# Kernel optimization log

Measured on AMD Instinct MI355X. Metric: run time of the kernel, lower is better.

Reference implementation:

```python
import jax, jax.numpy as jnp
import numpy as np

H, Mdim, C, P = 24, 48, 8, 8  # h = h_tilde, m = m_tilde, m_control, p


def setup_inputs() -> dict:
    key = jax.random.key(0)
    k = jax.random.split(key, 7)
    return {
        "y_rev": jax.random.normal(k[0], (2 * Mdim, P, 1), dtype=jnp.float32),  # y_rev[s] = y_nat_history[-(s+1)]
        "M_tilde": jax.random.normal(k[1], (H, Mdim, C, P), dtype=jnp.float32),
        "M": jax.random.normal(k[2], (H, Mdim, H, Mdim, C, P), dtype=jnp.float32),
        "sigma": jax.random.uniform(k[3], (H,), dtype=jnp.float32),      # positive Hankel eigenvalues
        "lambda_e": jax.random.uniform(k[4], (H,), dtype=jnp.float32),   # positive Hankel eigenvalues
        "phi": jax.random.normal(k[5], (Mdim, H), dtype=jnp.float32),
        "phi_tilde": jax.random.normal(k[6], (Mdim, H), dtype=jnp.float32),
    }


def reference(y_rev, M_tilde, M, sigma, lambda_e, phi, phi_tilde):
    m = phi.shape[0]
    lam4 = lambda_e ** 0.25  # [h]
    sig4 = sigma ** 0.25     # [h]
    y_m = y_rev[:m]          # [m, p, 1], y_m[j] = y_nat_history[-(j+1)]

    # term 0: M_tilde[0,0] @ y_t^nat
    u = M_tilde[0, 0] @ y_rev[0]  # [c, 1]

    # term 1: sum_ij lambda_i^{1/4} phi[j,i] (M_tilde[i,j] @ y_{t-j})
    c2 = lam4[:, None] * phi.T  # [h, m]
    u = u + jnp.einsum("ij,ijcp,jpq->cq", c2, M_tilde, y_m)

    # term 2: sum_lk sigma_l^{1/4} phi_tilde[k,l] (M[l,k,0,0] @ y_{t-k})
    c3 = sig4[:, None] * phi_tilde.T  # [h, m]
    u = u + jnp.einsum("lk,lkcp,kpq->cq", c3, M[:, :, 0, 0], y_m)

    # term 3: sum_ijlk (sigma_l lambda_i)^{1/4} phi_tilde[k,l] phi[j,i] (M[i,j,l,k] @ y_{t-j-k})
    c4 = jnp.einsum("i,l,ji,kl->ijlk", lam4, sig4, phi, phi_tilde)  # [h,m,h,m]
    idx = jnp.arange(m)[:, None] + jnp.arange(m)[None, :]           # offsets j+k in 0..2m-2
    y_jk = y_rev[idx]  # [m, m, p, 1]; y_jk[j,k] = y_nat_history[-(j+k+1)]
    u = u + jnp.einsum("ijlk,ijlkcp,jkpq->cq", c4, M, y_jk)
    return u
```

## Files before the change

kernel.cpp:

```cpp
#include <hip/hip_runtime.h>

#define HH 24
#define MM 48
#define CC 8
#define PP 8
#define IJ (HH * MM)
#define NBLK (IJ * IJ)

__global__ __launch_bounds__(256) void
dsc_big(const float* __restrict__ M,
        const float* __restrict__ y_rev,
        const float* __restrict__ sigma,
        const float* __restrict__ lambda_e,
        const float* __restrict__ phi,
        const float* __restrict__ phi_tilde,
        float* __restrict__ out)
{
    __shared__ float A[IJ];
    __shared__ float B[IJ];
    __shared__ float4 y4[2 * MM * 2];
    __shared__ float red[256];

    const int tid = threadIdx.x;

    for (int t = tid; t < IJ; t += 256) {
        int i = t / MM;
        int j = t - i * MM;
        A[t] = sqrtf(sqrtf(lambda_e[i])) * phi[j * HH + i];
        B[t] = sqrtf(sqrtf(sigma[i]))    * phi_tilde[j * HH + i];
    }
    const float4* yg = (const float4*)y_rev;
    for (int t = tid; t < 2 * MM * 2; t += 256) y4[t] = yg[t];
    __syncthreads();

    const int pos = tid & 15;
    const int ph  = pos & 1;
    const unsigned group   = (blockIdx.x * 256u + tid) >> 4;
    const unsigned nGroups = gridDim.x * 16u;

    const float4* M4 = (const float4*)M;
    float acc = 0.0f;
    for (unsigned b = group; b < NBLK; b += nGroups) {
        unsigned ij = b / IJ;
        unsigned lk = b - ij * IJ;
        unsigned j  = ij % MM;
        unsigned k  = lk % MM;
        float w = A[ij] * B[lk];
        float4 mv = M4[(size_t)b * 16u + pos];
        float4 yv = y4[(j + k) * 2u + ph];
        acc += w * (mv.x * yv.x + mv.y * yv.y + mv.z * yv.z + mv.w * yv.w);
    }

    red[tid] = acc;
    __syncthreads();
    if (tid < CC) {
        float s = 0.0f;
        #pragma unroll
        for (int g = 0; g < 16; ++g)
            s += red[g * 16 + tid * 2] + red[g * 16 + tid * 2 + 1];
        atomicAdd(out + tid, s);
    }
}

__global__ __launch_bounds__(256) void
dsc_small(const float* __restrict__ M,
          const float* __restrict__ M_tilde,
          const float* __restrict__ y_rev,
          const float* __restrict__ sigma,
          const float* __restrict__ lambda_e,
          const float* __restrict__ phi,
          const float* __restrict__ phi_tilde,
          float* __restrict__ out)
{
    __shared__ float A[IJ];
    __shared__ float B[IJ];
    __shared__ float4 y4[MM * 2];
    __shared__ float red[256];

    const int tid = threadIdx.x;
    for (int t = tid; t < IJ; t += 256) {
        int i = t / MM;
        int j = t - i * MM;
        A[t] = sqrtf(sqrtf(lambda_e[i])) * phi[j * HH + i];
        B[t] = sqrtf(sqrtf(sigma[i]))    * phi_tilde[j * HH + i];
    }
    const float4* yg = (const float4*)y_rev;
    for (int t = tid; t < MM * 2; t += 256) y4[t] = yg[t];
    __syncthreads();

    const int group = tid >> 4;
    const int pos   = tid & 15;
    const int ph    = pos & 1;

    const float4* Mt4 = (const float4*)M_tilde;
    const float4* M4  = (const float4*)M;

    float acc = 0.0f;
    for (int b = group; b < IJ; b += 16) {
        int j = b % MM;
        float4 mv = Mt4[b * 16 + pos];
        float4 yv = y4[j * 2 + ph];
        acc += A[b] * (mv.x * yv.x + mv.y * yv.y + mv.z * yv.z + mv.w * yv.w);
    }
    for (int b = group; b < IJ; b += 16) {
        int k = b % MM;
        float4 mv = M4[(size_t)b * 18432u + pos];
        float4 yv = y4[k * 2 + ph];
        acc += B[b] * (mv.x * yv.x + mv.y * yv.y + mv.z * yv.z + mv.w * yv.w);
    }
    if (group == 0) {
        float4 mv = Mt4[pos];
        float4 yv = y4[ph];
        acc += (mv.x * yv.x + mv.y * yv.y + mv.z * yv.z + mv.w * yv.w);
    }

    red[tid] = acc;
    __syncthreads();
    if (tid < CC) {
        float s = 0.0f;
        #pragma unroll
        for (int g = 0; g < 16; ++g)
            s += red[g * 16 + tid * 2] + red[g * 16 + tid * 2 + 1];
        atomicAdd(out + tid, s);
    }
}

extern "C" void kernel_launch(void* const* d_in, const int* in_sizes, int n_in,
                              void* d_out, int out_size, void* d_ws, size_t ws_size,
                              hipStream_t stream)
{
    const float* y_rev     = (const float*)d_in[0];
    const float* M_tilde   = (const float*)d_in[1];
    const float* M         = (const float*)d_in[2];
    const float* sigma     = (const float*)d_in[3];
    const float* lambda_e  = (const float*)d_in[4];
    const float* phi       = (const float*)d_in[5];
    const float* phi_tilde = (const float*)d_in[6];
    float* out = (float*)d_out;

    hipMemsetAsync(out, 0, out_size * sizeof(float), stream);

    dsc_small<<<1, 256, 0, stream>>>(M, M_tilde, y_rev, sigma, lambda_e,
                                     phi, phi_tilde, out);
    dsc_big<<<2048, 256, 0, stream>>>(M, y_rev, sigma, lambda_e,
                                      phi, phi_tilde, out);
}
```

Measured before the change: 532.4 us.

## Fuse small terms into main kernel and replace atomics with two-stage reduction

Merges the single-block kernel for terms 0-2 into the large streaming kernel by giving that work to spare groups in the first 1152 blocks. Each thread now handles one full output row (two float4 loads) instead of half a row. Per-block partial sums go to a workspace and a separate reduce kernel sums them, which removes the memset and the atomics. The goal is to drop the serial single-block kernel and the launch overheads. The cost is a workspace round trip and an extra launch, and the main loop is still bound by memory bandwidth on the 42 MB M tensor.

Measured after the change: 462.6 us. 13.1% less time.

```diff
diff --git a/kernel.cpp b/kernel.cpp
--- a/kernel.cpp
+++ b/kernel.cpp
@@ -6,49 +6,83 @@
 #define PP 8
 #define IJ (HH * MM)
 #define NBLK (IJ * IJ)
+#define GRID_BIG 2048
+#define TPB 256
+#define GROUPS_PER_BLOCK (TPB / 8)
+#define NGROUPS (GRID_BIG * GROUPS_PER_BLOCK)
 
-__global__ __launch_bounds__(256) void
-dsc_big(const float* __restrict__ M,
-        const float* __restrict__ y_rev,
-        const float* __restrict__ sigma,
-        const float* __restrict__ lambda_e,
-        const float* __restrict__ phi,
-        const float* __restrict__ phi_tilde,
-        float* __restrict__ out)
+__device__ __forceinline__ float dot4(const float4 a, const float4 b) {
+    return a.x * b.x + a.y * b.y + a.z * b.z + a.w * b.w;
+}
+
+__global__ __launch_bounds__(TPB) void
+dsc_main(const float* __restrict__ M,
+         const float* __restrict__ M_tilde,
+         const float* __restrict__ y_rev,
+         const float* __restrict__ sigma,
+         const float* __restrict__ lambda_e,
+         const float* __restrict__ phi,
+         const float* __restrict__ phi_tilde,
+         float* __restrict__ ws)
 {
     __shared__ float A[IJ];
     __shared__ float B[IJ];
     __shared__ float4 y4[2 * MM * 2];
-    __shared__ float red[256];
+    __shared__ float red[TPB];
 
     const int tid = threadIdx.x;
+    const int bid = blockIdx.x;
 
-    for (int t = tid; t < IJ; t += 256) {
+    for (int t = tid; t < IJ; t += TPB) {
         int i = t / MM;
         int j = t - i * MM;
         A[t] = sqrtf(sqrtf(lambda_e[i])) * phi[j * HH + i];
         B[t] = sqrtf(sqrtf(sigma[i]))    * phi_tilde[j * HH + i];
     }
     const float4* yg = (const float4*)y_rev;
-    for (int t = tid; t < 2 * MM * 2; t += 256) y4[t] = yg[t];
+    for (int t = tid; t < 2 * MM * 2; t += TPB) y4[t] = yg[t];
     __syncthreads();
 
-    const int pos = tid & 15;
-    const int ph  = pos & 1;
-    const unsigned group   = (blockIdx.x * 256u + tid) >> 4;
-    const unsigned nGroups = gridDim.x * 16u;
+    const int q = tid & 7;
+    const unsigned group   = ((unsigned)bid * TPB + tid) >> 3;
 
-    const float4* M4 = (const float4*)M;
+    const float4* M4  = (const float4*)M;
+    const float4* Mt4 = (const float4*)M_tilde;
+
     float acc = 0.0f;
-    for (unsigned b = group; b < NBLK; b += nGroups) {
+    for (unsigned b = group; b < NBLK; b += NGROUPS) {
         unsigned ij = b / IJ;
         unsigned lk = b - ij * IJ;
         unsigned j  = ij % MM;
         unsigned k  = lk % MM;
         float w = A[ij] * B[lk];
-        float4 mv = M4[(size_t)b * 16u + pos];
-        float4 yv = y4[(j + k) * 2u + ph];
-        acc += w * (mv.x * yv.x + mv.y * yv.y + mv.z * yv.z + mv.w * yv.w);
+        size_t base = (size_t)b * 16u + (unsigned)(q * 2);
+        float4 m0 = M4[base];
+        float4 m1 = M4[base + 1];
+        unsigned yr = (j + k) * 2u;
+        acc += w * (dot4(m0, y4[yr]) + dot4(m1, y4[yr + 1]));
+    }
+
+    if (bid < IJ) {
+        const int g = tid >> 3;
+        if (g == 0) {
+            unsigned j = (unsigned)bid % MM;
+            size_t base = (size_t)bid * 16u + (unsigned)(q * 2);
+            float4 m0 = Mt4[base];
+            float4 m1 = Mt4[base + 1];
+            acc += A[bid] * (dot4(m0, y4[j * 2]) + dot4(m1, y4[j * 2 + 1]));
+        } else if (g == 1) {
+            unsigned k = (unsigned)bid % MM;
+            size_t base = (size_t)bid * 1152u * 16u + (unsigned)(q * 2);
+            float4 m0 = M4[base];
+            float4 m1 = M4[base + 1];
+            acc += B[bid] * (dot4(m0, y4[k * 2]) + dot4(m1, y4[k * 2 + 1]));
+        } else if (g == 2 && bid == 0) {
+            size_t base = (unsigned)(q * 2);
+            float4 m0 = Mt4[base];
+            float4 m1 = Mt4[base + 1];
+            acc += dot4(m0, y4[0]) + dot4(m1, y4[1]);
+        }
     }
 
     red[tid] = acc;
@@ -56,72 +90,46 @@
     if (tid < CC) {
         float s = 0.0f;
         #pragma unroll
-        for (int g = 0; g < 16; ++g)
-            s += red[g * 16 + tid * 2] + red[g * 16 + tid * 2 + 1];
-        atomicAdd(out + tid, s);
+        for (int g = 0; g < GROUPS_PER_BLOCK; ++g)
+            s += red[g * 8 + tid];
+        ws[(size_t)bid * CC + tid] = s;
     }
 }
 
-__global__ __launch_bounds__(256) void
-dsc_small(const float* __restrict__ M,
-          const float* __restrict__ M_tilde,
-          const float* __restrict__ y_rev,
-          const float* __restrict__ sigma,
-          const float* __restrict__ lambda_e,
-          const float* __restrict__ phi,
-          const float* __restrict__ phi_tilde,
-          float* __restrict__ out)
+__global__ __launch_bounds__(TPB) void
+dsc_reduce(const float* __restrict__ ws, float* __restrict__ out)
 {
-    __shared__ float A[IJ];
-    __shared__ float B[IJ];
-    __shared__ float4 y4[MM * 2];
-    __shared__ float red[256];
+    __shared__ float4 redE[TPB];
+    __shared__ float4 redO[TPB];
 
     const int tid = threadIdx.x;
-    for (int t = tid; t < IJ; t += 256) {
-        int i = t / MM;
-        int j = t - i * MM;
-        A[t] = sqrtf(sqrtf(lambda_e[i])) * phi[j * HH + i];
-        B[t] = sqrtf(sqrtf(sigma[i]))    * phi_tilde[j * HH + i];
+    const float4* w4 = (const float4*)ws;
+
+    float4 accE = make_float4(0.f, 0.f, 0.f, 0.f);
+    float4 accO = make_float4(0.f, 0.f, 0.f, 0.f);
+    #pragma unroll
+    for (int u = 0; u < 16; u += 2) {
+        float4 e = w4[tid * 16 + u];
+        float4 o = w4[tid * 16 + u + 1];
+        accE.x += e.x; accE.y += e.y; accE.z += e.z; accE.w += e.w;
+        accO.x += o.x; accO.y += o.y; accO.z += o.z; accO.w += o.w;
     }
-    const float4* yg = (const float4*)y_rev;
-    for (int t = tid; t < MM * 2; t += 256) y4[t] = yg[t];
+    redE[tid] = accE;
+    redO[tid] = accO;
     __syncthreads();
-
-    const int group = tid >> 4;
-    const int pos   = tid & 15;
-    const int ph    = pos & 1;
-
-    const float4* Mt4 = (const float4*)M_tilde;
-    const float4* M4  = (const float4*)M;
-
-    float acc = 0.0f;
-    for (int b = group; b < IJ; b += 16) {
-        int j = b % MM;
-        float4 mv = Mt4[b * 16 + pos];
-        float4 yv = y4[j * 2 + ph];
-        acc += A[b] * (mv.x * yv.x + mv.y * yv.y + mv.z * yv.z + mv.w * yv.w);
+    for (int s = TPB / 2; s > 0; s >>= 1) {
+        if (tid < s) {
+            float4 a = redE[tid], b = redE[tid + s];
+            redE[tid] = make_float4(a.x + b.x, a.y + b.y, a.z + b.z, a.w + b.w);
+            a = redO[tid]; b = redO[tid + s];
+            redO[tid] = make_float4(a.x + b.x, a.y + b.y, a.z + b.z, a.w + b.w);
+        }
+        __syncthreads();
     }
-    for (int b = group; b < IJ; b += 16) {
-        int k = b % MM;
-        float4 mv = M4[(size_t)b * 18432u + pos];
-        float4 yv = y4[k * 2 + ph];
-        acc += B[b] * (mv.x * yv.x + mv.y * yv.y + mv.z * yv.z + mv.w * yv.w);
-    }
-    if (group == 0) {
-        float4 mv = Mt4[pos];
-        float4 yv = y4[ph];
-        acc += (mv.x * yv.x + mv.y * yv.y + mv.z * yv.z + mv.w * yv.w);
-    }
-
-    red[tid] = acc;
-    __syncthreads();
-    if (tid < CC) {
-        float s = 0.0f;
-        #pragma unroll
-        for (int g = 0; g < 16; ++g)
-            s += red[g * 16 + tid * 2] + red[g * 16 + tid * 2 + 1];
-        atomicAdd(out + tid, s);
+    if (tid == 0) {
+        float4 e = redE[0], o = redO[0];
+        out[0] = e.x; out[1] = e.y; out[2] = e.z; out[3] = e.w;
+        out[4] = o.x; out[5] = o.y; out[6] = o.z; out[7] = o.w;
     }
 }
 
@@ -137,11 +145,9 @@
     const float* phi       = (const float*)d_in[5];
     const float* phi_tilde = (const float*)d_in[6];
     float* out = (float*)d_out;
+    float* ws  = (float*)d_ws;
 
-    hipMemsetAsync(out, 0, out_size * sizeof(float), stream);
-
-    dsc_small<<<1, 256, 0, stream>>>(M, M_tilde, y_rev, sigma, lambda_e,
-                                     phi, phi_tilde, out);
-    dsc_big<<<2048, 256, 0, stream>>>(M, y_rev, sigma, lambda_e,
-                                      phi, phi_tilde, out);
+    dsc_main<<<GRID_BIG, TPB, 0, stream>>>(M, M_tilde, y_rev, sigma, lambda_e,
+                                           phi, phi_tilde, ws);
+    dsc_reduce<<<1, TPB, 0, stream>>>(ws, out);
 }
```
